# Performance work log

Measured on AMD Instinct MI355X. Metric: run time of the kernel, lower is better.

Reference implementation:

```python
import jax, jax.numpy as jnp
import numpy as np

N, M, D = 8192, 8192, 512

def setup_inputs() -> dict:
    key = jax.random.key(0)
    k1, k2 = jax.random.split(key)
    z = jax.random.normal(k1, (N, D), dtype=jnp.float32)
    e = jax.random.normal(k2, (M, D), dtype=jnp.float32)
    log_sigma = jnp.zeros((1,), dtype=jnp.float32)  # init_log_sigma = 0.0
    return {"z": z, "e": e, "log_sigma": log_sigma}

def reference(z, e, log_sigma):
    # Pairwise squared Euclidean distance via expansion (avoids NxMxD intermediate):
    # ||z_i - e_j||^2 = ||z_i||^2 + ||e_j||^2 - 2 z_i . e_j
    T = 1.0  # default temperature
    n, d = z.shape
    z2 = jnp.sum(z * z, axis=1)[:, None]          # (N,1)
    e2 = jnp.sum(e * e, axis=1)[None, :]          # (1,M)
    dist = z2 + e2 - 2.0 * jnp.einsum('nd,md->nm', z, e)  # (N,M) squared distances
    alpha = -1.0 / (2.0 * jnp.exp(log_sigma[0]) ** 2)
    lse = jax.scipy.special.logsumexp(alpha * dist / T, axis=0)  # (M,) reduce over N
    loss = -jnp.mean(T * lse)
    # 0.5 * z_dim * (2*log_sigma - log(e)) + log(N); log(e) == 1
    loss = loss + 0.5 * d * (2.0 * log_sigma[0] - 1.0) + jnp.log(jnp.float32(n))
    return loss
```

## Files before the change

kernel.cpp:

```cpp
#include <hip/hip_runtime.h>
#include <hip/hip_bf16.h>

#define N_PTS 8192
#define M_PTS 8192
#define DIM   512
#define NB    (N_PTS/256)

typedef __attribute__((ext_vector_type(8))) short bf8_t;
typedef __attribute__((ext_vector_type(8))) unsigned short us8_t;
typedef __attribute__((ext_vector_type(4))) float f4_t;

constexpr size_t ZB_OFF   = 0;
constexpr size_t EB_OFF   = (size_t)N_PTS * DIM * 2;
constexpr size_t Z2_OFF   = EB_OFF + (size_t)M_PTS * DIM * 2;
constexpr size_t E2_OFF   = Z2_OFF + (size_t)N_PTS * 4;
constexpr size_t PMAX_OFF = E2_OFF + (size_t)M_PTS * 4;
constexpr size_t PSUM_OFF = PMAX_OFF + (size_t)NB * M_PTS * 4;
constexpr size_t SUM_OFF  = PSUM_OFF + (size_t)NB * M_PTS * 4;
constexpr size_t CNT_OFF  = SUM_OFF + 8;

__device__ __forceinline__ unsigned short f2bf(float x) {
  __hip_bfloat16 h = __float2bfloat16(x);
  return __builtin_bit_cast(unsigned short, h);
}

__device__ __forceinline__ void gload_lds16(const void* g, void* l) {
  __builtin_amdgcn_global_load_lds(
      (const __attribute__((address_space(1))) unsigned int*)g,
      (__attribute__((address_space(3))) unsigned int*)l, 16, 0, 0);
}

#define BAR()         __builtin_amdgcn_s_barrier()
#define SFENCE()      __builtin_amdgcn_sched_barrier(0)
#define WAIT_LGKM0()  asm volatile("s_waitcnt lgkmcnt(0)" ::: "memory")
#define WAIT_VM0()    asm volatile("s_waitcnt vmcnt(0)" ::: "memory")

__global__ __launch_bounds__(256) void conv_kernel(const float* __restrict__ z,
                                                   const float* __restrict__ e,
                                                   char* __restrict__ ws) {
  const int tid = threadIdx.x;
  const int g = blockIdx.x * 4 + (tid >> 6);
  const bool isE = g >= N_PTS;
  const int row = isE ? (g - N_PTS) : g;
  const float* src = (isE ? e : z) + (size_t)row * DIM;
  char* panels = ws + (isE ? EB_OFF : ZB_OFF);
  float* rowsq = (float*)(ws + (isE ? E2_OFF : Z2_OFF));

  if (g == 0 && tid == 0) {
    *(double*)(ws + SUM_OFF) = 0.0;
    *(int*)(ws + CNT_OFF) = 0;
  }

  const int idx = tid & 63;
  float4 v0 = ((const float4*)src)[idx * 2];
  float4 v1 = ((const float4*)src)[idx * 2 + 1];
  float ss = v0.x*v0.x + v0.y*v0.y + v0.z*v0.z + v0.w*v0.w
           + v1.x*v1.x + v1.y*v1.y + v1.z*v1.z + v1.w*v1.w;

  us8_t bv;
  bv[0] = f2bf(v0.x); bv[1] = f2bf(v0.y); bv[2] = f2bf(v0.z); bv[3] = f2bf(v0.w);
  bv[4] = f2bf(v1.x); bv[5] = f2bf(v1.y); bv[6] = f2bf(v1.z); bv[7] = f2bf(v1.w);

  const int pi = (row >> 7) * 8 + (idx >> 3);
  const int r = row & 127;
  const int c16 = (idx & 7) * 16;
  const int byteoff = (r * 128 + c16) ^ ((r & 7) << 4);
  *(us8_t*)(panels + (size_t)pi * 16384 + byteoff) = bv;

  #pragma unroll
  for (int mk = 32; mk >= 1; mk >>= 1) ss += __shfl_xor(ss, mk, 64);
  if (idx == 0) rowsq[row] = ss;
}

__global__ __launch_bounds__(512, 2) void gemm_lse_kernel(char* __restrict__ ws,
                                                          const float* __restrict__ log_sigma) {
  __shared__ char lds[131072] __attribute__((aligned(16)));

  const int tid  = threadIdx.x;
  const int lane = tid & 63;
  const int wv   = tid >> 6;
  const int wr   = wv >> 2;
  const int wc   = wv & 3;

  const int bid  = blockIdx.x;
  const int x    = bid & 7;
  const int q    = bid >> 3;
  const int w    = q >> 5;
  const int s    = q & 31;
  const int rect = w * 8 + x;
  const int nblk = (rect & 3) * 8 + (s & 7);
  const int mblk = (rect >> 2) * 4 + (s >> 3);

  const char* zb = ws + ZB_OFF;
  const char* eb = ws + EB_OFF;
  const char* pb0 = zb + (size_t)(nblk * 16) * 16384;
  const char* pb1 = zb + (size_t)(nblk * 16 + 8) * 16384;
  const char* pb2 = eb + (size_t)(mblk * 16) * 16384;
  const char* pb3 = eb + (size_t)(mblk * 16 + 8) * 16384;
  const char* mypanel = (wv >> 1) == 0 ? pb0 : (wv >> 1) == 1 ? pb1 : (wv >> 1) == 2 ? pb2 : pb3;
  const int stage_goff = (wv & 1) * 8192 + lane * 16;
  const int stage_loff = (wv >> 1) * 16384 + (wv & 1) * 8192;

#define STAGE4(cur, kb, h) do { \
    _Pragma("unroll") \
    for (int i_ = 0; i_ < 4; ++i_) \
      gload_lds16(mypanel + (size_t)(kb) * 16384 + stage_goff + ((h) * 4 + i_) * 1024, \
                  lds + (cur) * 65536 + stage_loff + ((h) * 4 + i_) * 1024); \
  } while (0)

  const int rl  = lane & 15;
  const int kq  = (lane >> 4) * 16;
  const int swz = (rl & 7) << 4;
  const int adyn0 = rl * 128 + (kq ^ swz);
  const int adyn1 = rl * 128 + ((64 + kq) ^ swz);

  bf8_t fA[4][2];
  bf8_t fB[2][2][2];
  f4_t acc[8][4] = {};

#define READ_A(ih, cur) do { \
    _Pragma("unroll") \
    for (int f_ = 0; f_ < 4; ++f_) { \
      fA[f_][0] = *(const bf8_t*)(lds + (cur) * 65536 + wr * 16384 + (ih) * 8192 + f_ * 2048 + adyn0); \
      fA[f_][1] = *(const bf8_t*)(lds + (cur) * 65536 + wr * 16384 + (ih) * 8192 + f_ * 2048 + adyn1); \
    } \
  } while (0)

#define READ_B(jh, cur) do { \
    _Pragma("unroll") \
    for (int jf_ = 0; jf_ < 2; ++jf_) { \
      const int ub_ = (cur) * 65536 + 32768 + (wc >> 1) * 16384 + (wc & 1) * 8192 + ((jh) * 2 + jf_) * 2048; \
      fB[jh][jf_][0] = *(const bf8_t*)(lds + ub_ + adyn0); \
      fB[jh][jf_][1] = *(const bf8_t*)(lds + ub_ + adyn1); \
    } \
  } while (0)

#define MFMA_Q(ih, jh) do { \
    __builtin_amdgcn_s_setprio(1); \
    _Pragma("unroll") \
    for (int ks_ = 0; ks_ < 2; ++ks_) \
      _Pragma("unroll") \
      for (int i_ = 0; i_ < 4; ++i_) \
        _Pragma("unroll") \
        for (int jf_ = 0; jf_ < 2; ++jf_) \
          acc[(ih) * 4 + i_][(jh) * 2 + jf_] = __builtin_amdgcn_mfma_f32_16x16x32_bf16( \
              fA[i_][ks_], fB[jh][jf_][ks_], acc[(ih) * 4 + i_][(jh) * 2 + jf_], 0, 0, 0); \
    __builtin_amdgcn_s_setprio(0); \
  } while (0)

  STAGE4(0, 0, 0); STAGE4(0, 0, 1);
  WAIT_VM0(); SFENCE(); BAR(); SFENCE();

  for (int kb = 0; kb < 8; ++kb) {
    const int cur = kb & 1;
    READ_A(0, cur);
    READ_B(0, cur);
    if (kb + 1 < 8) STAGE4(cur ^ 1, kb + 1, 0);
    BAR(); WAIT_LGKM0(); SFENCE();
    MFMA_Q(0, 0);
    BAR();
    READ_B(1, cur);
    if (kb + 1 < 8) STAGE4(cur ^ 1, kb + 1, 1);
    BAR(); WAIT_LGKM0(); SFENCE();
    MFMA_Q(0, 1);
    BAR();
    READ_A(1, cur);
    BAR(); WAIT_LGKM0(); SFENCE();
    MFMA_Q(1, 0);
    BAR();
    MFMA_Q(1, 1);
    WAIT_VM0(); SFENCE(); BAR(); SFENCE();
  }

#undef STAGE4
#undef READ_A
#undef READ_B
#undef MFMA_Q

  const float lsv = log_sigma[0];
  const float sc  = -0.5f * __expf(-2.0f * lsv);
  const float n2s = -2.0f * sc;

  float z2v[8][4];
  {
    const float* z2p = (const float*)(ws + Z2_OFF) + nblk * 256 + wr * 128 + ((lane >> 4) << 2);
    #pragma unroll
    for (int i = 0; i < 8; ++i)
      #pragma unroll
      for (int r = 0; r < 4; ++r) z2v[i][r] = z2p[i * 16 + r];
  }
  float e2v[4];
  {
    const float* e2p = (const float*)(ws + E2_OFF) + mblk * 256 + wc * 64 + rl;
    #pragma unroll
    for (int j = 0; j < 4; ++j) e2v[j] = e2p[j * 16];
  }

  float* lmax = (float*)lds;
  float* lsum = (float*)(lds + 2048);

  #pragma unroll
  for (int j = 0; j < 4; ++j) {
    float mx = -1e30f;
    #pragma unroll
    for (int i = 0; i < 8; ++i)
      #pragma unroll
      for (int r = 0; r < 4; ++r) {
        float v = fmaf(n2s, acc[i][j][r], sc * (z2v[i][r] + e2v[j]));
        acc[i][j][r] = v;
        mx = fmaxf(mx, v);
      }
    float sm = 0.0f;
    #pragma unroll
    for (int i = 0; i < 8; ++i)
      #pragma unroll
      for (int r = 0; r < 4; ++r) sm += __expf(acc[i][j][r] - mx);

    #pragma unroll
    for (int mk = 16; mk <= 32; mk <<= 1) {
      float om = __shfl_xor(mx, mk, 64);
      float os = __shfl_xor(sm, mk, 64);
      float nm = fmaxf(mx, om);
      sm = sm * __expf(mx - nm) + os * __expf(om - nm);
      mx = nm;
    }
    if (lane < 16) {
      const int col = wc * 64 + j * 16 + lane;
      lmax[wr * 256 + col] = mx;
      lsum[wr * 256 + col] = sm;
    }
  }
  __syncthreads();

  if (tid < 256) {
    const float m0 = lmax[tid],       s0 = lsum[tid];
    const float m1 = lmax[256 + tid], s1 = lsum[256 + tid];
    const float Mx = fmaxf(m0, m1);
    const float S  = s0 * __expf(m0 - Mx) + s1 * __expf(m1 - Mx);
    float* pmax = (float*)(ws + PMAX_OFF);
    float* psum = (float*)(ws + PSUM_OFF);
    const size_t idx = (size_t)nblk * M_PTS + mblk * 256 + tid;
    pmax[idx] = Mx;
    psum[idx] = S;
  }
}

__global__ __launch_bounds__(256) void combine_finalize_kernel(char* __restrict__ ws,
                                                               const float* __restrict__ log_sigma,
                                                               float* __restrict__ out) {
  const int m = blockIdx.x * 256 + threadIdx.x;
  const float* pmax = (const float*)(ws + PMAX_OFF);
  const float* psum = (const float*)(ws + PSUM_OFF);
  float Mx = pmax[m];
  float S  = psum[m];
  #pragma unroll
  for (int nb = 1; nb < NB; ++nb) {
    const float pm = pmax[(size_t)nb * M_PTS + m];
    const float ps = psum[(size_t)nb * M_PTS + m];
    const float nm = fmaxf(Mx, pm);
    S = S * __expf(Mx - nm) + ps * __expf(pm - nm);
    Mx = nm;
  }
  double lse = (double)Mx + (double)logf(S);

  #pragma unroll
  for (int mk = 32; mk >= 1; mk >>= 1) lse += __shfl_xor(lse, mk, 64);
  __shared__ double red[4];
  if ((threadIdx.x & 63) == 0) red[threadIdx.x >> 6] = lse;
  __syncthreads();
  if (threadIdx.x == 0) {
    const double part = red[0] + red[1] + red[2] + red[3];
    double* sum = (double*)(ws + SUM_OFF);
    int* cnt = (int*)(ws + CNT_OFF);
    atomicAdd(sum, part);
    __threadfence();
    const int old = atomicAdd(cnt, 1);
    if (old == (M_PTS / 256) - 1) {
      const double total = atomicAdd(sum, 0.0);
      const double ls = (double)log_sigma[0];
      const double loss = -total / (double)M_PTS
                          + 0.5 * (double)DIM * (2.0 * ls - 1.0)
                          + log((double)N_PTS);
      out[0] = (float)loss;
    }
  }
}

extern "C" void kernel_launch(void* const* d_in, const int* in_sizes, int n_in,
                              void* d_out, int out_size, void* d_ws, size_t ws_size,
                              hipStream_t stream) {
  const float* z  = (const float*)d_in[0];
  const float* e  = (const float*)d_in[1];
  const float* ls = (const float*)d_in[2];
  float* out = (float*)d_out;
  char* ws = (char*)d_ws;

  conv_kernel<<<(N_PTS + M_PTS) / 4, 256, 0, stream>>>(z, e, ws);
  gemm_lse_kernel<<<(M_PTS / 256) * (N_PTS / 256), 512, 0, stream>>>(ws, ls);
  combine_finalize_kernel<<<M_PTS / 256, 256, 0, stream>>>(ws, ls, out);
}
```

Before: 151.2 us.

## Stage LDS panels in consumption order with partial vmcnt waits

Global-to-LDS staging is reorganized so that all 256 threads load one 16 KB panel at a time. The four panels are issued in the order they are consumed (A-half0, B-half1, B-half0, A-half1), and the end-of-iteration full vmcnt(0) drain is replaced by partial vmcnt waits. This is meant to overlap the next tile's loads with the remaining MFMA phases instead of stalling on every load at the end of each k-block. It also fully unrolls the k loop. The panel ordering against the waitcnt counts is delicate, and a wrong count could introduce a race on the double buffer.

```diff
diff --git a/kernel.cpp b/kernel.cpp
--- a/kernel.cpp
+++ b/kernel.cpp
@@ -33,6 +33,8 @@
 #define BAR()         __builtin_amdgcn_s_barrier()
 #define SFENCE()      __builtin_amdgcn_sched_barrier(0)
 #define WAIT_LGKM0()  asm volatile("s_waitcnt lgkmcnt(0)" ::: "memory")
+#define WAIT_VM4()    asm volatile("s_waitcnt vmcnt(4)" ::: "memory")
+#define WAIT_VM2()    asm volatile("s_waitcnt vmcnt(2)" ::: "memory")
 #define WAIT_VM0()    asm volatile("s_waitcnt vmcnt(0)" ::: "memory")
 
 __global__ __launch_bounds__(256) void conv_kernel(const float* __restrict__ z,
@@ -97,15 +99,12 @@
   const char* pb1 = zb + (size_t)(nblk * 16 + 8) * 16384;
   const char* pb2 = eb + (size_t)(mblk * 16) * 16384;
   const char* pb3 = eb + (size_t)(mblk * 16 + 8) * 16384;
-  const char* mypanel = (wv >> 1) == 0 ? pb0 : (wv >> 1) == 1 ? pb1 : (wv >> 1) == 2 ? pb2 : pb3;
-  const int stage_goff = (wv & 1) * 8192 + lane * 16;
-  const int stage_loff = (wv >> 1) * 16384 + (wv & 1) * 8192;
-
-#define STAGE4(cur, kb, h) do { \
-    _Pragma("unroll") \
-    for (int i_ = 0; i_ < 4; ++i_) \
-      gload_lds16(mypanel + (size_t)(kb) * 16384 + stage_goff + ((h) * 4 + i_) * 1024, \
-                  lds + (cur) * 65536 + stage_loff + ((h) * 4 + i_) * 1024); \
+
+#define STAGE2R(dstbuf, kb1, regoff, panel) do { \
+    gload_lds16((panel) + (size_t)(kb1) * 16384 + tid * 16, \
+                lds + (dstbuf) * 65536 + (regoff) + tid * 16); \
+    gload_lds16((panel) + (size_t)(kb1) * 16384 + 8192 + tid * 16, \
+                lds + (dstbuf) * 65536 + (regoff) + 8192 + tid * 16); \
   } while (0)
 
   const int rl  = lane & 15;
@@ -121,8 +120,8 @@
 #define READ_A(ih, cur) do { \
     _Pragma("unroll") \
     for (int f_ = 0; f_ < 4; ++f_) { \
-      fA[f_][0] = *(const bf8_t*)(lds + (cur) * 65536 + wr * 16384 + (ih) * 8192 + f_ * 2048 + adyn0); \
-      fA[f_][1] = *(const bf8_t*)(lds + (cur) * 65536 + wr * 16384 + (ih) * 8192 + f_ * 2048 + adyn1); \
+      fA[f_][0] = *(const bf8_t*)(lds + (cur) * 65536 + (ih) * 16384 + wr * 0 + f_ * 2048 + ((ih) == 99 ? 0 : 0) + adyn0 + 0); \
+      fA[f_][1] = *(const bf8_t*)(lds + (cur) * 65536 + (ih) * 16384 + f_ * 2048 + adyn1); \
     } \
   } while (0)
 
@@ -148,31 +147,54 @@
     __builtin_amdgcn_s_setprio(0); \
   } while (0)
 
-  STAGE4(0, 0, 0); STAGE4(0, 0, 1);
-  WAIT_VM0(); SFENCE(); BAR(); SFENCE();
-
+
+#undef READ_A
+#define READ_A(ih, cur) do { \
+    _Pragma("unroll") \
+    for (int f_ = 0; f_ < 4; ++f_) { \
+      const int ua_ = (cur) * 65536 + wr * 16384 + (ih) * 8192 + f_ * 2048; \
+      fA[f_][0] = *(const bf8_t*)(lds + ua_ + adyn0); \
+      fA[f_][1] = *(const bf8_t*)(lds + ua_ + adyn1); \
+    } \
+  } while (0)
+
+  STAGE2R(0, 0, 0,     pb0);
+  STAGE2R(0, 0, 49152, pb3);
+  STAGE2R(0, 0, 32768, pb2);
+  STAGE2R(0, 0, 16384, pb1);
+  WAIT_VM2(); SFENCE(); BAR(); SFENCE();
+
+  #pragma unroll
   for (int kb = 0; kb < 8; ++kb) {
     const int cur = kb & 1;
+    const int nxt = cur ^ 1;
+    const bool st = (kb < 7);
     READ_A(0, cur);
     READ_B(0, cur);
-    if (kb + 1 < 8) STAGE4(cur ^ 1, kb + 1, 0);
+    if (st) STAGE2R(nxt, kb + 1, 0, pb0);
     BAR(); WAIT_LGKM0(); SFENCE();
     MFMA_Q(0, 0);
     BAR();
     READ_B(1, cur);
-    if (kb + 1 < 8) STAGE4(cur ^ 1, kb + 1, 1);
+    if (st) { STAGE2R(nxt, kb + 1, 49152, pb3); WAIT_VM4(); }
+    else    { WAIT_VM0(); }
+    SFENCE();
     BAR(); WAIT_LGKM0(); SFENCE();
     MFMA_Q(0, 1);
     BAR();
     READ_A(1, cur);
+    if (st) STAGE2R(nxt, kb + 1, 32768, pb2);
     BAR(); WAIT_LGKM0(); SFENCE();
     MFMA_Q(1, 0);
     BAR();
+    if (st) { STAGE2R(nxt, kb + 1, 16384, pb1); WAIT_VM2(); }
+    SFENCE();
+    BAR(); SFENCE();
     MFMA_Q(1, 1);
-    WAIT_VM0(); SFENCE(); BAR(); SFENCE();
-  }
-
-#undef STAGE4
+    BAR();
+  }
+
+#undef STAGE2R
 #undef READ_A
 #undef READ_B
 #undef MFMA_Q
```

New measurement: 149.9 us. About the same (-0.8%).
